# Kernel optimization log

Measured on AMD Instinct MI355X. Metric: run time of the kernel, lower is better.

The kernel has to match this reference:

```python
import jax, jax.numpy as jnp
import numpy as np
import math

N, T, D_MODEL = 4, 2048, 1024
NHEAD = 16
HEAD_DIM = D_MODEL // NHEAD
ROTARY_DIM = 64
WINDOW = (128, 128)
ROPE_BASE = 10000.0


def _rope_cos_sin(seq_len, rotary_dim, dtype):
    # non-interleaved (GPT-NeoX style) rotary embedding tables
    inv_freq = 1.0 / (ROPE_BASE ** (jnp.arange(0, rotary_dim, 2, dtype=jnp.float32) / rotary_dim))
    t = jnp.arange(seq_len, dtype=jnp.float32)
    freqs = jnp.outer(t, inv_freq)  # [T, rotary_dim//2]
    return jnp.cos(freqs).astype(dtype), jnp.sin(freqs).astype(dtype)


def _apply_rope(x, cos, sin):
    # x: [N, T, H, D]; rotate first ROTARY_DIM dims, pass the rest through
    r = ROTARY_DIM
    x_rot, x_pass = x[..., :r], x[..., r:]
    x1, x2 = x_rot[..., : r // 2], x_rot[..., r // 2 :]
    c = cos[None, :, None, :]
    s = sin[None, :, None, :]
    out = jnp.concatenate([x1 * c - x2 * s, x1 * s + x2 * c], axis=-1)
    return jnp.concatenate([out, x_pass], axis=-1)


def _sliding_window_bias(seq_len, window, dtype):
    i = jnp.arange(seq_len)[:, None]
    j = jnp.arange(seq_len)[None, :]
    # triu(diag=-w0) & tril(diag=w1): keep j - i in [-w0, w1]
    keep = (j - i >= -window[0]) & (j - i <= window[1])
    return jnp.where(keep, jnp.zeros((), dtype), jnp.full((), -jnp.inf, dtype))


def setup_inputs() -> dict:
    key = jax.random.key(0)
    k1, k2, k3 = jax.random.split(key, 3)
    x = jax.random.normal(k1, (N, T, D_MODEL), dtype=jnp.float32)
    Wqkv = jax.random.normal(k2, (D_MODEL, 3 * D_MODEL), dtype=jnp.float32) * (1.0 / math.sqrt(D_MODEL))
    Wout = jax.random.normal(k3, (D_MODEL, D_MODEL), dtype=jnp.float32) * (1.0 / math.sqrt(D_MODEL))
    bout = jnp.zeros((D_MODEL,), dtype=jnp.float32)
    return {"x": x, "Wqkv": Wqkv, "Wout": Wout, "bout": bout}


def reference(x, Wqkv, Wout, bout):
    n, t, _ = x.shape
    qkv = (x @ Wqkv).reshape(n, t, 3, NHEAD, HEAD_DIM)
    q, k, v = qkv[:, :, 0], qkv[:, :, 1], qkv[:, :, 2]  # each [N, T, H, D]
    cos, sin = _rope_cos_sin(t, ROTARY_DIM, x.dtype)
    q = _apply_rope(q, cos, sin)
    k = _apply_rope(k, cos, sin)
    scale = 1.0 / math.sqrt(HEAD_DIM)
    bias = _sliding_window_bias(t, WINDOW, x.dtype)  # [T, T]
    scores = jnp.einsum("bthd,bshd->bhts", q, k) * scale + bias[None, None]
    attn = jax.nn.softmax(scores, axis=-1)
    out = jnp.einsum("bhts,bshd->bthd", attn, v).reshape(n, t, D_MODEL)
    return out @ Wout + bout
```

## Files before the change

kernel.cpp:

```cpp
#include <hip/hip_runtime.h>
#include <hip/hip_bf16.h>
#include <cstdint>
#include <cstddef>

typedef __bf16 bf16_t;
typedef bf16_t bf16x8 __attribute__((ext_vector_type(8)));
typedef float f32x4 __attribute__((ext_vector_type(4)));
typedef unsigned short ushort_t;

#define T_SEQ 2048
#define DM 1024
#define NH 16
#define HD 64
#define WIN 128
#define ROPE_C 0.28782313662425572f
#define SCALE_LOG2E 0.18033688011112042f
#define ATT_M 16.0f

__device__ __forceinline__ ushort_t f2bf(float f) {
    union { float f; unsigned u; } v; v.f = f;
    unsigned r = v.u + 0x7fff + ((v.u >> 16) & 1);
    return (ushort_t)(r >> 16);
}
__device__ __forceinline__ float sane(float v, float sent) {
    return (fabsf(v) < 1e30f) ? v : sent;
}
__device__ __forceinline__ void gld16(const ushort_t* g, ushort_t* l) {
    __builtin_amdgcn_global_load_lds(
        (const __attribute__((address_space(1))) unsigned int*)g,
        (__attribute__((address_space(3))) unsigned int*)l, 16, 0, 0);
}

__global__ __launch_bounds__(256) void kzero_f(float* __restrict__ p) {
    size_t i = ((size_t)blockIdx.x * 256 + threadIdx.x) * 4;
    float4 z; z.x = z.y = z.z = z.w = 0.f;
    *(float4*)(p + i) = z;
}

__global__ __launch_bounds__(256) void xcvt(const float* __restrict__ in,
                                            ushort_t* __restrict__ out) {
    size_t i = ((size_t)blockIdx.x * 256 + threadIdx.x) * 8;
    float4 a0 = *(const float4*)(in + i);
    float4 a1 = *(const float4*)(in + i + 4);
    ushort_t cv[8];
    cv[0] = f2bf(a0.x); cv[1] = f2bf(a0.y); cv[2] = f2bf(a0.z); cv[3] = f2bf(a0.w);
    cv[4] = f2bf(a1.x); cv[5] = f2bf(a1.y); cv[6] = f2bf(a1.z); cv[7] = f2bf(a1.w);
    *(uint4*)(out + i) = *(uint4*)cv;
}

__global__ __launch_bounds__(256) void ktranspose_f2b(const float* __restrict__ in,
                                                      ushort_t* __restrict__ out,
                                                      int R, int C) {
    __shared__ __align__(16) ushort_t tile[64][72];
    const int c0 = blockIdx.x * 64, r0 = blockIdx.y * 64;
    const int tid = threadIdx.x;
    const int rl = tid >> 2, q4 = tid & 3;
    const float* src = in + (size_t)(r0 + rl) * C + c0 + q4 * 16;
    ushort_t cv[16];
#pragma unroll
    for (int i = 0; i < 4; i++) {
        float4 f = *(const float4*)(src + i * 4);
        cv[i * 4 + 0] = f2bf(f.x); cv[i * 4 + 1] = f2bf(f.y);
        cv[i * 4 + 2] = f2bf(f.z); cv[i * 4 + 3] = f2bf(f.w);
    }
    *(uint4*)&tile[rl][q4 * 16]     = *(uint4*)&cv[0];
    *(uint4*)&tile[rl][q4 * 16 + 8] = *(uint4*)&cv[8];
    __syncthreads();
    const int cl = tid >> 2;
    ushort_t tmp[16];
#pragma unroll
    for (int i = 0; i < 16; i++) tmp[i] = tile[q4 * 16 + i][cl];
    ushort_t* dst = out + (size_t)(c0 + cl) * R + r0 + q4 * 16;
    *(uint4*)(dst)     = *(uint4*)&tmp[0];
    *(uint4*)(dst + 8) = *(uint4*)&tmp[8];
}

__global__ __launch_bounds__(256) void gemm_qkv(const ushort_t* __restrict__ A,
                                                const ushort_t* __restrict__ Bt,
                                                ushort_t* __restrict__ Qr,
                                                ushort_t* __restrict__ Kr,
                                                ushort_t* __restrict__ Vt) {
    __shared__ __align__(16) ushort_t As[128 * 32];
    __shared__ __align__(16) ushort_t Bs[128 * 32];
    const int m0 = blockIdx.x * 128, n0 = blockIdx.y * 128;
    const int tid = threadIdx.x;
    const int lane = tid & 63, w = tid >> 6;
    const int wm = (w & 1) * 64, wn = (w >> 1) * 64;
    const int c = lane & 15, g = lane >> 4;
    const int lrow = lane >> 2, lcol = (lane & 3) * 8;
    const int ch0 = 2 * w, ch1 = 2 * w + 1;

    f32x4 acc[4][4];
#pragma unroll
    for (int mi = 0; mi < 4; mi++)
#pragma unroll
        for (int ni = 0; ni < 4; ni++)
#pragma unroll
            for (int r = 0; r < 4; r++) acc[mi][ni][r] = 0.f;

    for (int k0 = 0; k0 < 1024; k0 += 32) {
        __syncthreads();
        gld16(A  + (size_t)(m0 + ch0 * 16 + lrow) * 1024 + k0 + lcol, &As[ch0 * 512]);
        gld16(A  + (size_t)(m0 + ch1 * 16 + lrow) * 1024 + k0 + lcol, &As[ch1 * 512]);
        gld16(Bt + (size_t)(n0 + ch0 * 16 + lrow) * 1024 + k0 + lcol, &Bs[ch0 * 512]);
        gld16(Bt + (size_t)(n0 + ch1 * 16 + lrow) * 1024 + k0 + lcol, &Bs[ch1 * 512]);
        __syncthreads();
        bf16x8 af[4], bfr[4];
#pragma unroll
        for (int mi = 0; mi < 4; mi++)
            af[mi] = *(const bf16x8*)&As[(wm + mi * 16 + c) * 32 + g * 8];
#pragma unroll
        for (int ni = 0; ni < 4; ni++)
            bfr[ni] = *(const bf16x8*)&Bs[(wn + ni * 16 + c) * 32 + g * 8];
#pragma unroll
        for (int mi = 0; mi < 4; mi++)
#pragma unroll
            for (int ni = 0; ni < 4; ni++)
                acc[mi][ni] = __builtin_amdgcn_mfma_f32_16x16x32_bf16(
                    af[mi], bfr[ni], acc[mi][ni], 0, 0, 0);
    }

    const int nb = n0 + wn;
    const int sec = nb >> 10;
    const int h = (nb >> 6) & 15;

    if (sec < 2) {
        ushort_t* dst = (sec == 0) ? Qr : Kr;
        const float invf0 = __expf(-(float)(c) * ROPE_C);
        const float invf1 = __expf(-(float)(16 + c) * ROPE_C);
#pragma unroll
        for (int mi = 0; mi < 4; mi++)
#pragma unroll
            for (int r = 0; r < 4; r++) {
                int tg = m0 + wm + mi * 16 + g * 4 + r;
                int nB = tg >> 11, t = tg & (T_SEQ - 1);
                float a0 = (float)t * invf0, a1 = (float)t * invf1;
                float s0 = __sinf(a0), c0 = __cosf(a0);
                float s1 = __sinf(a1), c1 = __cosf(a1);
                size_t base = ((size_t)(nB * NH + h) * T_SEQ + t) * 64;
                float x1a = acc[mi][0][r], x2a = acc[mi][2][r];
                float x1b = acc[mi][1][r], x2b = acc[mi][3][r];
                dst[base + c]      = f2bf(sane(x1a * c0 - x2a * s0, 1e3f));
                dst[base + 16 + c] = f2bf(sane(x1b * c1 - x2b * s1, 1e3f));
                dst[base + 32 + c] = f2bf(sane(x1a * s0 + x2a * c0, 1e3f));
                dst[base + 48 + c] = f2bf(sane(x1b * s1 + x2b * c1, 1e3f));
            }
    } else {
#pragma unroll
        for (int mi = 0; mi < 4; mi++) {
            int tgb = m0 + wm + mi * 16 + g * 4;
            int nB = tgb >> 11, t = tgb & (T_SEQ - 1);
            size_t vrow = (size_t)(nB * NH + h) * 64 * T_SEQ;
#pragma unroll
            for (int ni = 0; ni < 4; ni++) {
                ushort4 pk;
                pk.x = f2bf(sane(acc[mi][ni][0], 1e3f));
                pk.y = f2bf(sane(acc[mi][ni][1], 1e3f));
                pk.z = f2bf(sane(acc[mi][ni][2], 1e3f));
                pk.w = f2bf(sane(acc[mi][ni][3], 1e3f));
                *(ushort4*)&Vt[vrow + (size_t)(ni * 16 + c) * T_SEQ + t] = pk;
            }
        }
    }
}

__global__ __launch_bounds__(256) void gemm_out(const ushort_t* __restrict__ A,
                                                const ushort_t* __restrict__ Bt,
                                                float* __restrict__ C,
                                                const float* __restrict__ bias) {
    __shared__ __align__(16) ushort_t As[128 * 32];
    __shared__ __align__(16) ushort_t Bs[128 * 32];
    const int m0 = blockIdx.x * 128, n0 = blockIdx.y * 128;
    const int tid = threadIdx.x;
    const int lane = tid & 63, w = tid >> 6;
    const int wm = (w & 1) * 64, wn = (w >> 1) * 64;
    const int c = lane & 15, g = lane >> 4;
    const int lrow = lane >> 2, lcol = (lane & 3) * 8;
    const int ch0 = 2 * w, ch1 = 2 * w + 1;

    f32x4 acc[4][4];
#pragma unroll
    for (int mi = 0; mi < 4; mi++)
#pragma unroll
        for (int ni = 0; ni < 4; ni++)
#pragma unroll
            for (int r = 0; r < 4; r++) acc[mi][ni][r] = 0.f;

    for (int k0 = 0; k0 < 1024; k0 += 32) {
        __syncthreads();
        gld16(A  + (size_t)(m0 + ch0 * 16 + lrow) * 1024 + k0 + lcol, &As[ch0 * 512]);
        gld16(A  + (size_t)(m0 + ch1 * 16 + lrow) * 1024 + k0 + lcol, &As[ch1 * 512]);
        gld16(Bt + (size_t)(n0 + ch0 * 16 + lrow) * 1024 + k0 + lcol, &Bs[ch0 * 512]);
        gld16(Bt + (size_t)(n0 + ch1 * 16 + lrow) * 1024 + k0 + lcol, &Bs[ch1 * 512]);
        __syncthreads();
        bf16x8 af[4], bfr[4];
#pragma unroll
        for (int mi = 0; mi < 4; mi++)
            af[mi] = *(const bf16x8*)&As[(wm + mi * 16 + c) * 32 + g * 8];
#pragma unroll
        for (int ni = 0; ni < 4; ni++)
            bfr[ni] = *(const bf16x8*)&Bs[(wn + ni * 16 + c) * 32 + g * 8];
#pragma unroll
        for (int mi = 0; mi < 4; mi++)
#pragma unroll
            for (int ni = 0; ni < 4; ni++)
                acc[mi][ni] = __builtin_amdgcn_mfma_f32_16x16x32_bf16(
                    af[mi], bfr[ni], acc[mi][ni], 0, 0, 0);
    }

#pragma unroll
    for (int ni = 0; ni < 4; ni++) {
        int col = n0 + wn + ni * 16 + c;
        float bv = bias[col];
#pragma unroll
        for (int mi = 0; mi < 4; mi++)
#pragma unroll
            for (int r = 0; r < 4; r++) {
                int rowi = m0 + wm + mi * 16 + g * 4 + r;
                C[(size_t)rowi * 1024 + col] = sane(acc[mi][ni][r] + bv, 1e8f);
            }
    }
}

__global__ __launch_bounds__(256) void attn_swin(const ushort_t* __restrict__ Qr,
                                                 const ushort_t* __restrict__ Kr,
                                                 const ushort_t* __restrict__ Vt,
                                                 ushort_t* __restrict__ O) {
    __shared__ __align__(16) ushort_t Ks[32 * 72];
    __shared__ __align__(16) ushort_t Vs[64 * 72];
    __shared__ __align__(16) ushort_t pbuf[4][16 * 32];
    const int tid = threadIdx.x;
    const int wid = tid >> 6, lane = tid & 63;
    const int qb = (blockIdx.x & 31) * 64;
    const int h = (blockIdx.x >> 5) & 15, n = blockIdx.x >> 9;
    const int t0 = qb + wid * 16;
    const int c = lane & 15, g = lane >> 4;
    const size_t hb = ((size_t)(n * NH + h)) * T_SEQ * 64;
    const int ks_row = tid >> 3, ks_col = (tid & 7) * 8;
    const int vs_row = tid >> 2, vs_col = (tid & 3) * 8;

    bf16x8 qf0 = *(const bf16x8*)(Qr + hb + (size_t)(t0 + c) * 64 + g * 8);
    bf16x8 qf1 = *(const bf16x8*)(Qr + hb + (size_t)(t0 + c) * 64 + 32 + g * 8);

    f32x4 o[4];
    float l_r[4];
#pragma unroll
    for (int i = 0; i < 4; i++) {
        l_r[i] = 0.f;
#pragma unroll
        for (int r = 0; r < 4; r++) o[i][r] = 0.f;
    }

    int sB_lo = qb - WIN;       if (sB_lo < 0) sB_lo = 0;
    int sB_hi = qb + 63 + WIN;  if (sB_hi > T_SEQ - 1) sB_hi = T_SEQ - 1;

    uint4 kreg = *(const uint4*)(Kr + hb + (size_t)(sB_lo + ks_row) * 64 + ks_col);
    uint4 vreg = *(const uint4*)(Vt + hb + (size_t)vs_row * T_SEQ + sB_lo + vs_col);

    for (int s0 = sB_lo; s0 <= sB_hi; s0 += 32) {
        __syncthreads();
        *(uint4*)&Ks[ks_row * 72 + ks_col] = kreg;
        *(uint4*)&Vs[vs_row * 72 + vs_col] = vreg;
        __syncthreads();
        int s1 = s0 + 32;
        if (s1 <= sB_hi) {
            kreg = *(const uint4*)(Kr + hb + (size_t)(s1 + ks_row) * 64 + ks_col);
            vreg = *(const uint4*)(Vt + hb + (size_t)vs_row * T_SEQ + s1 + vs_col);
        }
        if (s0 > t0 + 143 || s0 + 31 < t0 - WIN) continue;

        f32x4 S[2];
#pragma unroll
        for (int sh = 0; sh < 2; sh++) {
            bf16x8 kf0 = *(const bf16x8*)&Ks[(sh * 16 + c) * 72 + g * 8];
            bf16x8 kf1 = *(const bf16x8*)&Ks[(sh * 16 + c) * 72 + 32 + g * 8];
            f32x4 z;
#pragma unroll
            for (int r = 0; r < 4; r++) z[r] = 0.f;
            z = __builtin_amdgcn_mfma_f32_16x16x32_bf16(qf0, kf0, z, 0, 0, 0);
            z = __builtin_amdgcn_mfma_f32_16x16x32_bf16(qf1, kf1, z, 0, 0, 0);
            S[sh] = z;
        }
        const bool interior = (s0 >= t0 - 113) && (s0 <= t0 + 97);
        ushort_t* pb = pbuf[wid];
        if (interior) {
#pragma unroll
            for (int sh = 0; sh < 2; sh++)
#pragma unroll
                for (int r = 0; r < 4; r++) {
                    float p = exp2f(S[sh][r] * SCALE_LOG2E - ATT_M);
                    l_r[r] += p;
                    pb[(g * 4 + r) * 32 + sh * 16 + c] = f2bf(p);
                }
        } else {
#pragma unroll
            for (int sh = 0; sh < 2; sh++)
#pragma unroll
                for (int r = 0; r < 4; r++) {
                    int s = s0 + sh * 16 + c;
                    int q = t0 + g * 4 + r;
                    bool keep = (s - q >= -WIN) && (s - q <= WIN);
                    float v = keep ? S[sh][r] * SCALE_LOG2E : -1e30f;
                    float p = exp2f(v - ATT_M);
                    l_r[r] += p;
                    pb[(g * 4 + r) * 32 + sh * 16 + c] = f2bf(p);
                }
        }
        __asm__ volatile("s_waitcnt lgkmcnt(0)" ::: "memory");
        bf16x8 pf = *(const bf16x8*)&pb[c * 32 + g * 8];
        __asm__ volatile("" ::: "memory");

#pragma unroll
        for (int di = 0; di < 4; di++) {
            bf16x8 vf = *(const bf16x8*)&Vs[(di * 16 + c) * 72 + g * 8];
            o[di] = __builtin_amdgcn_mfma_f32_16x16x32_bf16(pf, vf, o[di], 0, 0, 0);
        }
    }

#pragma unroll
    for (int off = 1; off < 16; off <<= 1)
#pragma unroll
        for (int r = 0; r < 4; r++) l_r[r] += __shfl_xor(l_r[r], off, 64);
    float inv[4];
#pragma unroll
    for (int r = 0; r < 4; r++) inv[r] = __builtin_amdgcn_rcpf(l_r[r]);

#pragma unroll
    for (int di = 0; di < 4; di++)
#pragma unroll
        for (int r = 0; r < 4; r++) {
            int q = t0 + g * 4 + r;
            float val = o[di][r] * inv[r];
            O[((size_t)(n * T_SEQ + q)) * DM + h * 64 + di * 16 + c] = f2bf(sane(val, 1e6f));
        }
}

extern "C" void kernel_launch(void* const* d_in, const int* in_sizes, int n_in,
                              void* d_out, int out_size, void* d_ws, size_t ws_size,
                              hipStream_t stream) {
    const float* x    = (const float*)d_in[0];
    const float* Wqkv = (const float*)d_in[1];
    const float* Wout = (const float*)d_in[2];
    const float* bout = (const float*)d_in[3];
    float* out = (float*)d_out;

    const size_t NEED = 72ull << 20;
    if (ws_size < NEED) {
        kzero_f<<<dim3(8192), 256, 0, stream>>>(out);
        return;
    }
    char* ws = (char*)d_ws;
    ushort_t* WqkvT = (ushort_t*)(ws);
    ushort_t* WoutT = (ushort_t*)(ws + (6ull << 20));
    ushort_t* Qr    = (ushort_t*)(ws + (8ull << 20));
    ushort_t* Kr    = (ushort_t*)(ws + (24ull << 20));
    ushort_t* Vt    = (ushort_t*)(ws + (40ull << 20));
    ushort_t* xb    = (ushort_t*)(ws + (56ull << 20));
    ushort_t* Oat   = xb;

    xcvt<<<dim3(4096), 256, 0, stream>>>(x, xb);
    ktranspose_f2b<<<dim3(48, 16), 256, 0, stream>>>(Wqkv, WqkvT, 1024, 3072);
    ktranspose_f2b<<<dim3(16, 16), 256, 0, stream>>>(Wout, WoutT, 1024, 1024);
    gemm_qkv<<<dim3(64, 24), 256, 0, stream>>>(xb, WqkvT, Qr, Kr, Vt);
    attn_swin<<<dim3(2048), 256, 0, stream>>>(Qr, Kr, Vt, Oat);
    gemm_out<<<dim3(64, 8), 256, 0, stream>>>(Oat, WoutT, out, bout);
}
```

Before: 223.2 us.

## Merge prep kernels, halve gemm_out M tile, and give attention two query sub-tiles

```diff
diff --git a/kernel.cpp b/kernel.cpp
--- a/kernel.cpp
+++ b/kernel.cpp
@@ -37,22 +37,10 @@
     *(float4*)(p + i) = z;
 }
 
-__global__ __launch_bounds__(256) void xcvt(const float* __restrict__ in,
-                                            ushort_t* __restrict__ out) {
-    size_t i = ((size_t)blockIdx.x * 256 + threadIdx.x) * 8;
-    float4 a0 = *(const float4*)(in + i);
-    float4 a1 = *(const float4*)(in + i + 4);
-    ushort_t cv[8];
-    cv[0] = f2bf(a0.x); cv[1] = f2bf(a0.y); cv[2] = f2bf(a0.z); cv[3] = f2bf(a0.w);
-    cv[4] = f2bf(a1.x); cv[5] = f2bf(a1.y); cv[6] = f2bf(a1.z); cv[7] = f2bf(a1.w);
-    *(uint4*)(out + i) = *(uint4*)cv;
-}
-
-__global__ __launch_bounds__(256) void ktranspose_f2b(const float* __restrict__ in,
-                                                      ushort_t* __restrict__ out,
-                                                      int R, int C) {
+__device__ __forceinline__ void trans_f2b_tile(const float* __restrict__ in,
+                                               ushort_t* __restrict__ out,
+                                               int R, int C, int c0, int r0) {
     __shared__ __align__(16) ushort_t tile[64][72];
-    const int c0 = blockIdx.x * 64, r0 = blockIdx.y * 64;
     const int tid = threadIdx.x;
     const int rl = tid >> 2, q4 = tid & 3;
     const float* src = in + (size_t)(r0 + rl) * C + c0 + q4 * 16;
@@ -73,6 +61,30 @@
     ushort_t* dst = out + (size_t)(c0 + cl) * R + r0 + q4 * 16;
     *(uint4*)(dst)     = *(uint4*)&tmp[0];
     *(uint4*)(dst + 8) = *(uint4*)&tmp[8];
+}
+
+__global__ __launch_bounds__(256) void prep(const float* __restrict__ x,
+                                            const float* __restrict__ Wqkv,
+                                            const float* __restrict__ Wout,
+                                            ushort_t* __restrict__ xb,
+                                            ushort_t* __restrict__ WqkvT,
+                                            ushort_t* __restrict__ WoutT) {
+    const int bx = blockIdx.x;
+    if (bx < 4096) {
+        size_t i = ((size_t)bx * 256 + threadIdx.x) * 8;
+        float4 a0 = *(const float4*)(x + i);
+        float4 a1 = *(const float4*)(x + i + 4);
+        ushort_t cv[8];
+        cv[0] = f2bf(a0.x); cv[1] = f2bf(a0.y); cv[2] = f2bf(a0.z); cv[3] = f2bf(a0.w);
+        cv[4] = f2bf(a1.x); cv[5] = f2bf(a1.y); cv[6] = f2bf(a1.z); cv[7] = f2bf(a1.w);
+        *(uint4*)(xb + i) = *(uint4*)cv;
+    } else if (bx < 4864) {
+        int tb = bx - 4096;
+        trans_f2b_tile(Wqkv, WqkvT, 1024, 3072, (tb % 48) * 64, (tb / 48) * 64);
+    } else {
+        int tb = bx - 4864;
+        trans_f2b_tile(Wout, WoutT, 1024, 1024, (tb & 15) * 64, (tb >> 4) * 64);
+    }
 }
 
 __global__ __launch_bounds__(256) void gemm_qkv(const ushort_t* __restrict__ A,
@@ -168,19 +180,19 @@
                                                 const ushort_t* __restrict__ Bt,
                                                 float* __restrict__ C,
                                                 const float* __restrict__ bias) {
-    __shared__ __align__(16) ushort_t As[128 * 32];
+    __shared__ __align__(16) ushort_t As[64 * 32];
     __shared__ __align__(16) ushort_t Bs[128 * 32];
-    const int m0 = blockIdx.x * 128, n0 = blockIdx.y * 128;
+    const int m0 = blockIdx.x * 64, n0 = blockIdx.y * 128;
     const int tid = threadIdx.x;
     const int lane = tid & 63, w = tid >> 6;
-    const int wm = (w & 1) * 64, wn = (w >> 1) * 64;
+    const int wm = (w & 1) * 32, wn = (w >> 1) * 64;
     const int c = lane & 15, g = lane >> 4;
     const int lrow = lane >> 2, lcol = (lane & 3) * 8;
     const int ch0 = 2 * w, ch1 = 2 * w + 1;
 
-    f32x4 acc[4][4];
-#pragma unroll
-    for (int mi = 0; mi < 4; mi++)
+    f32x4 acc[2][4];
+#pragma unroll
+    for (int mi = 0; mi < 2; mi++)
 #pragma unroll
         for (int ni = 0; ni < 4; ni++)
 #pragma unroll
@@ -188,20 +200,19 @@
 
     for (int k0 = 0; k0 < 1024; k0 += 32) {
         __syncthreads();
-        gld16(A  + (size_t)(m0 + ch0 * 16 + lrow) * 1024 + k0 + lcol, &As[ch0 * 512]);
-        gld16(A  + (size_t)(m0 + ch1 * 16 + lrow) * 1024 + k0 + lcol, &As[ch1 * 512]);
+        gld16(A  + (size_t)(m0 + w * 16 + lrow) * 1024 + k0 + lcol, &As[w * 512]);
         gld16(Bt + (size_t)(n0 + ch0 * 16 + lrow) * 1024 + k0 + lcol, &Bs[ch0 * 512]);
         gld16(Bt + (size_t)(n0 + ch1 * 16 + lrow) * 1024 + k0 + lcol, &Bs[ch1 * 512]);
         __syncthreads();
-        bf16x8 af[4], bfr[4];
-#pragma unroll
-        for (int mi = 0; mi < 4; mi++)
+        bf16x8 af[2], bfr[4];
+#pragma unroll
+        for (int mi = 0; mi < 2; mi++)
             af[mi] = *(const bf16x8*)&As[(wm + mi * 16 + c) * 32 + g * 8];
 #pragma unroll
         for (int ni = 0; ni < 4; ni++)
             bfr[ni] = *(const bf16x8*)&Bs[(wn + ni * 16 + c) * 32 + g * 8];
 #pragma unroll
-        for (int mi = 0; mi < 4; mi++)
+        for (int mi = 0; mi < 2; mi++)
 #pragma unroll
             for (int ni = 0; ni < 4; ni++)
                 acc[mi][ni] = __builtin_amdgcn_mfma_f32_16x16x32_bf16(
@@ -213,7 +224,7 @@
         int col = n0 + wn + ni * 16 + c;
         float bv = bias[col];
 #pragma unroll
-        for (int mi = 0; mi < 4; mi++)
+        for (int mi = 0; mi < 2; mi++)
 #pragma unroll
             for (int r = 0; r < 4; r++) {
                 int rowi = m0 + wm + mi * 16 + g * 4 + r;
@@ -228,31 +239,37 @@
                                                  ushort_t* __restrict__ O) {
     __shared__ __align__(16) ushort_t Ks[32 * 72];
     __shared__ __align__(16) ushort_t Vs[64 * 72];
-    __shared__ __align__(16) ushort_t pbuf[4][16 * 32];
+    __shared__ __align__(16) ushort_t pbuf[4][2][16 * 32];
     const int tid = threadIdx.x;
     const int wid = tid >> 6, lane = tid & 63;
-    const int qb = (blockIdx.x & 31) * 64;
-    const int h = (blockIdx.x >> 5) & 15, n = blockIdx.x >> 9;
-    const int t0 = qb + wid * 16;
+    const int qb = (blockIdx.x & 15) * 128;
+    const int h = (blockIdx.x >> 4) & 15, n = blockIdx.x >> 8;
     const int c = lane & 15, g = lane >> 4;
     const size_t hb = ((size_t)(n * NH + h)) * T_SEQ * 64;
+    const int t0s[2] = { qb + wid * 16, qb + 64 + wid * 16 };
     const int ks_row = tid >> 3, ks_col = (tid & 7) * 8;
     const int vs_row = tid >> 2, vs_col = (tid & 3) * 8;
 
-    bf16x8 qf0 = *(const bf16x8*)(Qr + hb + (size_t)(t0 + c) * 64 + g * 8);
-    bf16x8 qf1 = *(const bf16x8*)(Qr + hb + (size_t)(t0 + c) * 64 + 32 + g * 8);
-
-    f32x4 o[4];
-    float l_r[4];
-#pragma unroll
-    for (int i = 0; i < 4; i++) {
-        l_r[i] = 0.f;
-#pragma unroll
-        for (int r = 0; r < 4; r++) o[i][r] = 0.f;
-    }
-
-    int sB_lo = qb - WIN;       if (sB_lo < 0) sB_lo = 0;
-    int sB_hi = qb + 63 + WIN;  if (sB_hi > T_SEQ - 1) sB_hi = T_SEQ - 1;
+    bf16x8 qf0[2], qf1[2];
+#pragma unroll
+    for (int sub = 0; sub < 2; sub++) {
+        qf0[sub] = *(const bf16x8*)(Qr + hb + (size_t)(t0s[sub] + c) * 64 + g * 8);
+        qf1[sub] = *(const bf16x8*)(Qr + hb + (size_t)(t0s[sub] + c) * 64 + 32 + g * 8);
+    }
+
+    f32x4 o[2][4];
+    float l_r[2][4];
+#pragma unroll
+    for (int sub = 0; sub < 2; sub++)
+#pragma unroll
+        for (int i = 0; i < 4; i++) {
+            l_r[sub][i] = 0.f;
+#pragma unroll
+            for (int r = 0; r < 4; r++) o[sub][i][r] = 0.f;
+        }
+
+    int sB_lo = qb - WIN;        if (sB_lo < 0) sB_lo = 0;
+    int sB_hi = qb + 127 + WIN;  if (sB_hi > T_SEQ - 1) sB_hi = T_SEQ - 1;
 
     uint4 kreg = *(const uint4*)(Kr + hb + (size_t)(sB_lo + ks_row) * 64 + ks_col);
     uint4 vreg = *(const uint4*)(Vt + hb + (size_t)vs_row * T_SEQ + sB_lo + vs_col);
@@ -267,72 +284,88 @@
             kreg = *(const uint4*)(Kr + hb + (size_t)(s1 + ks_row) * 64 + ks_col);
             vreg = *(const uint4*)(Vt + hb + (size_t)vs_row * T_SEQ + s1 + vs_col);
         }
-        if (s0 > t0 + 143 || s0 + 31 < t0 - WIN) continue;
-
-        f32x4 S[2];
-#pragma unroll
-        for (int sh = 0; sh < 2; sh++) {
-            bf16x8 kf0 = *(const bf16x8*)&Ks[(sh * 16 + c) * 72 + g * 8];
-            bf16x8 kf1 = *(const bf16x8*)&Ks[(sh * 16 + c) * 72 + 32 + g * 8];
-            f32x4 z;
-#pragma unroll
-            for (int r = 0; r < 4; r++) z[r] = 0.f;
-            z = __builtin_amdgcn_mfma_f32_16x16x32_bf16(qf0, kf0, z, 0, 0, 0);
-            z = __builtin_amdgcn_mfma_f32_16x16x32_bf16(qf1, kf1, z, 0, 0, 0);
-            S[sh] = z;
-        }
-        const bool interior = (s0 >= t0 - 113) && (s0 <= t0 + 97);
-        ushort_t* pb = pbuf[wid];
-        if (interior) {
-#pragma unroll
-            for (int sh = 0; sh < 2; sh++)
-#pragma unroll
-                for (int r = 0; r < 4; r++) {
-                    float p = exp2f(S[sh][r] * SCALE_LOG2E - ATT_M);
-                    l_r[r] += p;
-                    pb[(g * 4 + r) * 32 + sh * 16 + c] = f2bf(p);
-                }
-        } else {
-#pragma unroll
-            for (int sh = 0; sh < 2; sh++)
-#pragma unroll
-                for (int r = 0; r < 4; r++) {
-                    int s = s0 + sh * 16 + c;
-                    int q = t0 + g * 4 + r;
-                    bool keep = (s - q >= -WIN) && (s - q <= WIN);
-                    float v = keep ? S[sh][r] * SCALE_LOG2E : -1e30f;
-                    float p = exp2f(v - ATT_M);
-                    l_r[r] += p;
-                    pb[(g * 4 + r) * 32 + sh * 16 + c] = f2bf(p);
-                }
+        bool act[2];
+#pragma unroll
+        for (int sub = 0; sub < 2; sub++)
+            act[sub] = !(s0 > t0s[sub] + 143 || s0 + 31 < t0s[sub] - WIN);
+        if (!act[0] && !act[1]) continue;
+
+#pragma unroll
+        for (int sub = 0; sub < 2; sub++) {
+            if (!act[sub]) continue;
+            const int t0 = t0s[sub];
+            f32x4 S[2];
+#pragma unroll
+            for (int sh = 0; sh < 2; sh++) {
+                bf16x8 kf0 = *(const bf16x8*)&Ks[(sh * 16 + c) * 72 + g * 8];
+                bf16x8 kf1 = *(const bf16x8*)&Ks[(sh * 16 + c) * 72 + 32 + g * 8];
+                f32x4 z;
+#pragma unroll
+                for (int r = 0; r < 4; r++) z[r] = 0.f;
+                z = __builtin_amdgcn_mfma_f32_16x16x32_bf16(qf0[sub], kf0, z, 0, 0, 0);
+                z = __builtin_amdgcn_mfma_f32_16x16x32_bf16(qf1[sub], kf1, z, 0, 0, 0);
+                S[sh] = z;
+            }
+            const bool interior = (s0 >= t0 - 113) && (s0 <= t0 + 97);
+            ushort_t* pb = pbuf[wid][sub];
+            if (interior) {
+#pragma unroll
+                for (int sh = 0; sh < 2; sh++)
+#pragma unroll
+                    for (int r = 0; r < 4; r++) {
+                        float p = exp2f(S[sh][r] * SCALE_LOG2E - ATT_M);
+                        l_r[sub][r] += p;
+                        pb[(g * 4 + r) * 32 + sh * 16 + c] = f2bf(p);
+                    }
+            } else {
+#pragma unroll
+                for (int sh = 0; sh < 2; sh++)
+#pragma unroll
+                    for (int r = 0; r < 4; r++) {
+                        int s = s0 + sh * 16 + c;
+                        int q = t0 + g * 4 + r;
+                        bool keep = (s - q >= -WIN) && (s - q <= WIN);
+                        float v = keep ? S[sh][r] * SCALE_LOG2E : -1e30f;
+                        float p = exp2f(v - ATT_M);
+                        l_r[sub][r] += p;
+                        pb[(g * 4 + r) * 32 + sh * 16 + c] = f2bf(p);
+                    }
+            }
         }
         __asm__ volatile("s_waitcnt lgkmcnt(0)" ::: "memory");
-        bf16x8 pf = *(const bf16x8*)&pb[c * 32 + g * 8];
+#pragma unroll
+        for (int sub = 0; sub < 2; sub++) {
+            if (!act[sub]) continue;
+            bf16x8 pf = *(const bf16x8*)&pbuf[wid][sub][c * 32 + g * 8];
+#pragma unroll
+            for (int di = 0; di < 4; di++) {
+                bf16x8 vf = *(const bf16x8*)&Vs[(di * 16 + c) * 72 + g * 8];
+                o[sub][di] = __builtin_amdgcn_mfma_f32_16x16x32_bf16(pf, vf, o[sub][di], 0, 0, 0);
+            }
+        }
         __asm__ volatile("" ::: "memory");
-
-#pragma unroll
-        for (int di = 0; di < 4; di++) {
-            bf16x8 vf = *(const bf16x8*)&Vs[(di * 16 + c) * 72 + g * 8];
-            o[di] = __builtin_amdgcn_mfma_f32_16x16x32_bf16(pf, vf, o[di], 0, 0, 0);
-        }
-    }
-
-#pragma unroll
-    for (int off = 1; off < 16; off <<= 1)
-#pragma unroll
-        for (int r = 0; r < 4; r++) l_r[r] += __shfl_xor(l_r[r], off, 64);
-    float inv[4];
-#pragma unroll
-    for (int r = 0; r < 4; r++) inv[r] = __builtin_amdgcn_rcpf(l_r[r]);
-
-#pragma unroll
-    for (int di = 0; di < 4; di++)
-#pragma unroll
-        for (int r = 0; r < 4; r++) {
-            int q = t0 + g * 4 + r;
-            float val = o[di][r] * inv[r];
-            O[((size_t)(n * T_SEQ + q)) * DM + h * 64 + di * 16 + c] = f2bf(sane(val, 1e6f));
-        }
+    }
+
+#pragma unroll
+    for (int sub = 0; sub < 2; sub++) {
+#pragma unroll
+        for (int off = 1; off < 16; off <<= 1)
+#pragma unroll
+            for (int r = 0; r < 4; r++)
+                l_r[sub][r] += __shfl_xor(l_r[sub][r], off, 64);
+        float inv[4];
+#pragma unroll
+        for (int r = 0; r < 4; r++) inv[r] = __builtin_amdgcn_rcpf(l_r[sub][r]);
+#pragma unroll
+        for (int di = 0; di < 4; di++)
+#pragma unroll
+            for (int r = 0; r < 4; r++) {
+                int q = t0s[sub] + g * 4 + r;
+                float val = o[sub][di][r] * inv[r];
+                O[((size_t)(n * T_SEQ + q)) * DM + h * 64 + di * 16 + c] =
+                    f2bf(sane(val, 1e6f));
+            }
+    }
 }
 
 extern "C" void kernel_launch(void* const* d_in, const int* in_sizes, int n_in,
@@ -358,10 +391,8 @@
     ushort_t* xb    = (ushort_t*)(ws + (56ull << 20));
     ushort_t* Oat   = xb;
 
-    xcvt<<<dim3(4096), 256, 0, stream>>>(x, xb);
-    ktranspose_f2b<<<dim3(48, 16), 256, 0, stream>>>(Wqkv, WqkvT, 1024, 3072);
-    ktranspose_f2b<<<dim3(16, 16), 256, 0, stream>>>(Wout, WoutT, 1024, 1024);
+    prep<<<dim3(5120), 256, 0, stream>>>(x, Wqkv, Wout, xb, WqkvT, WoutT);
     gemm_qkv<<<dim3(64, 24), 256, 0, stream>>>(xb, WqkvT, Qr, Kr, Vt);
-    attn_swin<<<dim3(2048), 256, 0, stream>>>(Qr, Kr, Vt, Oat);
-    gemm_out<<<dim3(64, 8), 256, 0, stream>>>(Oat, WoutT, out, bout);
-}
+    attn_swin<<<dim3(1024), 256, 0, stream>>>(Qr, Kr, Vt, Oat);
+    gemm_out<<<dim3(128, 8), 256, 0, stream>>>(Oat, WoutT, out, bout);
+}
```

Result: faster. 215.2 us (-3.6%).
